# Performance work log

Hardware: AMD Instinct MI355X
Metric: run time of the kernel (lower is better)

The kernel has to match this reference:

```python
import jax, jax.numpy as jnp
import numpy as np
from jax import lax

EMBED = 512
HEADS = 8
KD = EMBED // HEADS  # key_dim == head_dim (value_factor=1)


def setup_inputs() -> dict:
    key = jax.random.key(0)
    ks = jax.random.split(key, 13)
    b, h, w = 4, 128, 128
    s = 0.02
    return {
        "x": jax.random.normal(ks[0], (b, h, w, EMBED), jnp.float32),
        "mask_h": jax.random.normal(ks[1], (HEADS, h, h), jnp.float32),
        "mask_w": jax.random.normal(ks[2], (HEADS, w, w), jnp.float32),
        "Wq": jax.random.normal(ks[3], (EMBED, EMBED), jnp.float32) * s,
        "bq": jnp.zeros((EMBED,), jnp.float32),
        "Wk": jax.random.normal(ks[4], (EMBED, EMBED), jnp.float32) * s,
        "bk": jnp.zeros((EMBED,), jnp.float32),
        "Wv": jax.random.normal(ks[5], (EMBED, EMBED), jnp.float32) * s,
        "bv": jnp.zeros((EMBED,), jnp.float32),
        "lepe_w": jax.random.normal(ks[6], (5, 5, 1, EMBED), jnp.float32) * s,  # depthwise 5x5, HWIO
        "lepe_b": jnp.zeros((EMBED,), jnp.float32),
        "Wo": jax.random.normal(ks[7], (EMBED, EMBED), jnp.float32) * s,
        "bo": jnp.zeros((EMBED,), jnp.float32),
    }


def reference(x, mask_h, mask_w, Wq, bq, Wk, bk, Wv, bv, lepe_w, lepe_b, Wo, bo):
    b, h, w, _ = x.shape
    scaling = KD ** -0.5
    q = x @ Wq + bq                      # (b,h,w,C)
    k = (x @ Wk + bk) * scaling
    v = x @ Wv + bv

    # depthwise-conv positional term (LePE), 5x5 pad 2, groups=C
    lepe = lax.conv_general_dilated(
        v, lepe_w, window_strides=(1, 1), padding=[(2, 2), (2, 2)],
        dimension_numbers=("NHWC", "HWIO", "NHWC"), feature_group_count=EMBED,
    ) + lepe_b

    qr = q.reshape(b, h, w, HEADS, KD)
    kr = k.reshape(b, h, w, HEADS, KD)
    vr = v.reshape(b, h, w, HEADS, KD)

    # width-axis attention (per row), additive per-head decay mask
    sw = jnp.einsum("bhqnd,bhknd->bhnqk", qr, kr) + mask_w[None, None]  # (b,h,n,w,w)
    Aw = jax.nn.softmax(sw, axis=-1)
    o1 = jnp.einsum("bhnqk,bhknd->bhqnd", Aw, vr)                       # (b,h,w,n,d)

    # height-axis attention (per column) on the width-pass output
    sh = jnp.einsum("bqwnd,bkwnd->bwnqk", qr, kr) + mask_h[None, None]  # (b,w,n,h,h)
    Ah = jax.nn.softmax(sh, axis=-1)
    o2 = jnp.einsum("bwnqk,bkwnd->bqwnd", Ah, o1)                       # (b,h,w,n,d)

    out = o2.reshape(b, h, w, EMBED) + lepe
    return out @ Wo + bo
```

## Files before the change

### kernel.cpp

```cpp
#include <hip/hip_runtime.h>
#include <stdint.h>
#include <stddef.h>

typedef unsigned short u16;
typedef __attribute__((ext_vector_type(8))) short bf16x8;
typedef __attribute__((ext_vector_type(4))) float f32x4;

__device__ __forceinline__ u16 f2bf(float f) {
  union { float f; uint32_t u; } v; v.f = f;
  uint32_t u = v.u;
  return (u16)((u + 0x7FFFu + ((u >> 16) & 1u)) >> 16);
}
__device__ __forceinline__ float bf2f(u16 b) {
  union { uint32_t u; float f; } v; v.u = ((uint32_t)b) << 16;
  return v.f;
}

__device__ __forceinline__ void glds16(const u16* g, u16* l) {
  __builtin_amdgcn_global_load_lds((const __attribute__((address_space(1))) void*)g,
                                   (__attribute__((address_space(3))) void*)l, 16, 0, 0);
}

#define MFMA(a, b, c) __builtin_amdgcn_mfma_f32_16x16x32_bf16((a), (b), (c), 0, 0, 0)


__global__ __launch_bounds__(256) void k_cvt_bf16(const float* __restrict__ in,
                                                  u16* __restrict__ out, int n) {
  int i = (blockIdx.x * 256 + threadIdx.x) * 8;
  if (i >= n) return;
  const float4* p = (const float4*)(in + i);
  float4 a = p[0], b = p[1];
  union { bf16x8 v; u16 s[8]; } o;
  o.s[0] = f2bf(a.x); o.s[1] = f2bf(a.y); o.s[2] = f2bf(a.z); o.s[3] = f2bf(a.w);
  o.s[4] = f2bf(b.x); o.s[5] = f2bf(b.y); o.s[6] = f2bf(b.z); o.s[7] = f2bf(b.w);
  *(bf16x8*)(out + i) = o.v;
}


__global__ __launch_bounds__(256) void k_build_w(
    const float* __restrict__ Wq, const float* __restrict__ Wk,
    const float* __restrict__ Wv, const float* __restrict__ Wo,
    const float* __restrict__ bq, const float* __restrict__ bk,
    const float* __restrict__ bv,
    u16* __restrict__ wqkvT, u16* __restrict__ woT, float* __restrict__ bias)
{
  __shared__ u16 tl[64 * 73];
  const int bid = blockIdx.x;
  const int mtx = bid >> 6;
  const int tr = (bid >> 3) & 7, tc = bid & 7;
  const float* W = (mtx == 0) ? Wq : (mtx == 1) ? Wk : (mtx == 2) ? Wv : Wo;
  const float s = (mtx == 1) ? 0.125f : 1.0f;
  const int t = threadIdx.x;
  const int lr = t >> 6, lc = t & 63;
  #pragma unroll
  for (int it = 0; it < 16; ++it) {
    int k = tr * 64 + it * 4 + lr;
    int n = tc * 64 + lc;
    tl[lc * 73 + it * 4 + lr] = f2bf(W[(size_t)k * 512 + n] * s);
  }
  __syncthreads();
  u16* dst = (mtx == 3) ? woT : (wqkvT + (size_t)mtx * 512 * 512);
  #pragma unroll
  for (int it = 0; it < 16; ++it) {
    int n = tc * 64 + it * 4 + lr;
    int k = tr * 64 + lc;
    dst[(size_t)n * 512 + k] = tl[(it * 4 + lr) * 73 + lc];
  }
  if (bid < 6) {
    int i = bid * 256 + t;
    const float* B = (i < 512) ? bq : (i < 1024) ? bk : bv;
    float sc = (i >= 512 && i < 1024) ? 0.125f : 1.0f;
    bias[i] = B[i & 511] * sc;
  }
}


__device__ __forceinline__ void stageH(const u16* __restrict__ src, int ld, size_t grow0,
                                       int kt, int row0, u16* lmat, int t) {
  #pragma unroll
  for (int it = 0; it < 2; ++it) {
    int e = it * 4096 + t * 8;
    int row = row0 + (e >> 6);
    int ch = (e >> 3) & 7;
    int cs = ch ^ (row & 7);
    glds16(src + (grow0 + row) * (size_t)ld + kt * 64 + cs * 8, lmat + row * 64 + ch * 8);
  }
}

__device__ __forceinline__ bf16x8 ldfrag(const u16* lmat, int row, int c) {
  return *(const bf16x8*)(lmat + row * 64 + ((c ^ (row & 7)) << 3));
}

template<bool STAGE, bool VM8>
__device__ __forceinline__ void process_tile(
    const u16* __restrict__ A, int lda, size_t rowA0,
    const u16* __restrict__ BT, int ldb, size_t rowB0,
    u16* LAc, u16* LBc, int nxt,
    int wm, int wn, int fq, int fr, int t,
    f32x4 (&acc)[2][4][2][2])
{
  bf16x8 bA[4][2], bB[2][2][2];
  #pragma unroll
  for (int n = 0; n < 2; ++n)
    #pragma unroll
    for (int kk = 0; kk < 2; ++kk)
      bB[0][n][kk] = ldfrag(LBc, wn * 32 + n * 16 + fr, kk * 4 + fq);
  #pragma unroll
  for (int m = 0; m < 4; ++m)
    #pragma unroll
    for (int kk = 0; kk < 2; ++kk)
      bA[m][kk] = ldfrag(LAc, wm * 64 + m * 16 + fr, kk * 4 + fq);
  __builtin_amdgcn_s_setprio(1);
  #pragma unroll
  for (int m = 0; m < 4; ++m)
    #pragma unroll
    for (int n = 0; n < 2; ++n)
      #pragma unroll
      for (int kk = 0; kk < 2; ++kk)
        acc[0][m][0][n] = MFMA(bA[m][kk], bB[0][n][kk], acc[0][m][0][n]);
  __builtin_amdgcn_s_setprio(0);
  __builtin_amdgcn_s_barrier();
  #pragma unroll
  for (int n = 0; n < 2; ++n)
    #pragma unroll
    for (int kk = 0; kk < 2; ++kk)
      bB[1][n][kk] = ldfrag(LBc, 128 + wn * 32 + n * 16 + fr, kk * 4 + fq);
  if (STAGE) {
    stageH(A, lda, rowA0, nxt, 0, LAc, t);
    stageH(BT, ldb, rowB0, nxt, 0, LBc, t);
  }
  __builtin_amdgcn_s_setprio(1);
  #pragma unroll
  for (int m = 0; m < 4; ++m)
    #pragma unroll
    for (int n = 0; n < 2; ++n)
      #pragma unroll
      for (int kk = 0; kk < 2; ++kk)
        acc[0][m][1][n] = MFMA(bA[m][kk], bB[1][n][kk], acc[0][m][1][n]);
  __builtin_amdgcn_s_setprio(0);
  __builtin_amdgcn_s_barrier();
  #pragma unroll
  for (int m = 0; m < 4; ++m)
    #pragma unroll
    for (int kk = 0; kk < 2; ++kk)
      bA[m][kk] = ldfrag(LAc, 128 + wm * 64 + m * 16 + fr, kk * 4 + fq);
  if (STAGE) stageH(BT, ldb, rowB0, nxt, 128, LBc, t);
  __builtin_amdgcn_s_setprio(1);
  #pragma unroll
  for (int m = 0; m < 4; ++m)
    #pragma unroll
    for (int n = 0; n < 2; ++n)
      #pragma unroll
      for (int kk = 0; kk < 2; ++kk)
        acc[1][m][0][n] = MFMA(bA[m][kk], bB[0][n][kk], acc[1][m][0][n]);
  __builtin_amdgcn_s_setprio(0);
  __builtin_amdgcn_s_barrier();
  if (STAGE) stageH(A, lda, rowA0, nxt, 128, LAc, t);
  __builtin_amdgcn_s_setprio(1);
  #pragma unroll
  for (int m = 0; m < 4; ++m)
    #pragma unroll
    for (int n = 0; n < 2; ++n)
      #pragma unroll
      for (int kk = 0; kk < 2; ++kk)
        acc[1][m][1][n] = MFMA(bA[m][kk], bB[1][n][kk], acc[1][m][1][n]);
  __builtin_amdgcn_s_setprio(0);
  if (VM8) asm volatile("s_waitcnt vmcnt(8)" ::: "memory");
  else     asm volatile("s_waitcnt vmcnt(0)" ::: "memory");
  __builtin_amdgcn_s_barrier();
}

template<bool OUT_F32, int NTN>
__global__ __launch_bounds__(512, 2) void k_gemm256(
    const u16* __restrict__ A, int lda,
    const u16* __restrict__ BT, int ldb,
    const float* __restrict__ bias,
    void* __restrict__ Cp, int ldc)
{
  __shared__ u16 lds[65536];
  u16* LA0 = lds;
  u16* LB0 = lds + 16384;
  u16* LA1 = lds + 32768;
  u16* LB1 = lds + 49152;

  const int t = threadIdx.x, l = t & 63, w = t >> 6;
  const int wm = w >> 2, wn = w & 3;
  const int fq = l >> 4, fr = l & 15;

  const int bid = blockIdx.x;
  const int cpx = gridDim.x >> 3;
  const int swz = (bid & 7) * cpx + (bid >> 3);
  const int tn = swz % NTN, tm = swz / NTN;
  const size_t rowA0 = (size_t)tm * 256;
  const size_t rowB0 = (size_t)tn * 256;

  f32x4 acc[2][4][2][2];
  #pragma unroll
  for (int a = 0; a < 2; ++a)
    #pragma unroll
    for (int m = 0; m < 4; ++m)
      #pragma unroll
      for (int b = 0; b < 2; ++b)
        #pragma unroll
        for (int n = 0; n < 2; ++n) acc[a][m][b][n] = (f32x4){0.f, 0.f, 0.f, 0.f};

  stageH(A,  lda, rowA0, 0, 0,   LA0, t); stageH(A,  lda, rowA0, 0, 128, LA0, t);
  stageH(BT, ldb, rowB0, 0, 0,   LB0, t); stageH(BT, ldb, rowB0, 0, 128, LB0, t);
  stageH(A,  lda, rowA0, 1, 0,   LA1, t); stageH(A,  lda, rowA0, 1, 128, LA1, t);
  stageH(BT, ldb, rowB0, 1, 0,   LB1, t); stageH(BT, ldb, rowB0, 1, 128, LB1, t);
  asm volatile("s_waitcnt vmcnt(8)" ::: "memory");
  __builtin_amdgcn_s_barrier();

  for (int i = 0; i < 3; ++i) {
    process_tile<true, true>(A, lda, rowA0, BT, ldb, rowB0, LA0, LB0, 2 * i + 2,
                             wm, wn, fq, fr, t, acc);
    process_tile<true, true>(A, lda, rowA0, BT, ldb, rowB0, LA1, LB1, 2 * i + 3,
                             wm, wn, fq, fr, t, acc);
  }
  process_tile<false, false>(A, lda, rowA0, BT, ldb, rowB0, LA0, LB0, 0,
                             wm, wn, fq, fr, t, acc);
  process_tile<false, false>(A, lda, rowA0, BT, ldb, rowB0, LA1, LB1, 0,
                             wm, wn, fq, fr, t, acc);

  if (OUT_F32) {
    #pragma unroll
    for (int nh = 0; nh < 2; ++nh)
      #pragma unroll
      for (int n = 0; n < 2; ++n) {
        int col = (int)rowB0 + nh * 128 + wn * 32 + n * 16 + fr;
        float bb = bias[col];
        #pragma unroll
        for (int mh = 0; mh < 2; ++mh)
          #pragma unroll
          for (int m = 0; m < 4; ++m)
            #pragma unroll
            for (int r = 0; r < 4; ++r) {
              size_t row = rowA0 + mh * 128 + wm * 64 + m * 16 + fq * 4 + r;
              ((float*)Cp)[row * ldc + col] = acc[mh][m][nh][n][r] + bb;
            }
      }
  } else {
    #pragma unroll
    for (int mh = 0; mh < 2; ++mh) {
      #pragma unroll
      for (int nh = 0; nh < 2; ++nh)
        #pragma unroll
        for (int n = 0; n < 2; ++n) {
          int col = nh * 128 + wn * 32 + n * 16 + fr;
          float bb = bias[(int)rowB0 + col];
          #pragma unroll
          for (int m = 0; m < 4; ++m)
            #pragma unroll
            for (int r = 0; r < 4; ++r) {
              int row = wm * 64 + m * 16 + fq * 4 + r;
              int ch = (col >> 3) ^ (row & 7);
              lds[row * 256 + ch * 8 + (col & 7)] = f2bf(acc[mh][m][nh][n][r] + bb);
            }
        }
      __syncthreads();
      {
        int row = t >> 2, q = t & 3;
        #pragma unroll
        for (int j = 0; j < 8; ++j) {
          int ch = (q * 8 + j) ^ (row & 7);
          bf16x8 v = *(const bf16x8*)(lds + row * 256 + ch * 8);
          *(bf16x8*)((u16*)Cp + (rowA0 + mh * 128 + row) * (size_t)ldc
                     + rowB0 + q * 64 + j * 8) = v;
        }
      }
      __syncthreads();
    }
  }
}


__global__ __launch_bounds__(256) void k_lepe(
    const u16* __restrict__ qkv, const float* __restrict__ w5,
    const float* __restrict__ lb, u16* __restrict__ outp)
{
  __shared__ u16 wlds[12800];
  #pragma unroll
  for (int j = 0; j < 50; ++j) {
    int idx = j * 256 + threadIdx.x;
    wlds[idx] = f2bf(w5[idx]);
  }
  __syncthreads();

  const int t = threadIdx.x, w = t >> 6, l = t & 63;
  const int c0 = l << 3;
  const int bid = blockIdx.x;
  const int x = (bid & 31) * 4 + w;
  const int y0 = ((bid >> 5) & 15) * 8;
  const int b = bid >> 9;

  float acc[8][8];
  {
    float4 b0 = *(const float4*)(lb + c0);
    float4 b1 = *(const float4*)(lb + c0 + 4);
    #pragma unroll
    for (int tt = 0; tt < 8; ++tt) {
      acc[tt][0] = b0.x; acc[tt][1] = b0.y; acc[tt][2] = b0.z; acc[tt][3] = b0.w;
      acc[tt][4] = b1.x; acc[tt][5] = b1.y; acc[tt][6] = b1.z; acc[tt][7] = b1.w;
    }
  }

  #pragma unroll
  for (int r = 0; r < 12; ++r) {
    int yy = y0 + r - 2;
    if ((unsigned)yy < 128u) {
      #pragma unroll
      for (int dx = 0; dx < 5; ++dx) {
        int xx = x + dx - 2;
        if ((unsigned)xx < 128u) {
          union { bf16x8 v; u16 s[8]; } v8;
          v8.v = *(const bf16x8*)(qkv + (size_t)((b * 128 + yy) * 128 + xx) * 1536
                                  + 1024 + c0);
          float vf[8];
          #pragma unroll
          for (int j = 0; j < 8; ++j) vf[j] = bf2f(v8.s[j]);
          #pragma unroll
          for (int tt = 0; tt < 8; ++tt) {
            int dy = r - tt;
            if (dy >= 0 && dy <= 4) {
              union { bf16x8 v; u16 s[8]; } w8;
              w8.v = *(const bf16x8*)(wlds + (dy * 5 + dx) * 512 + c0);
              #pragma unroll
              for (int j = 0; j < 8; ++j)
                acc[tt][j] += vf[j] * bf2f(w8.s[j]);
            }
          }
        }
      }
    }
  }

  #pragma unroll
  for (int tt = 0; tt < 8; ++tt) {
    size_t tok = (size_t)(b * 128 + y0 + tt) * 128 + x;
    union { bf16x8 v; u16 s[8]; } ov;
    #pragma unroll
    for (int j = 0; j < 8; ++j) ov.s[j] = f2bf(acc[tt][j]);
    *(bf16x8*)(outp + tok * 512 + c0) = ov.v;
  }
}


template<int AXIS>
__global__ __launch_bounds__(512) void k_attn(
    const u16* qkv, const float* __restrict__ mask,
    const u16* __restrict__ lepe, u16* outp)
{
  __shared__ u16 smem[24576];
  u16* q_s = smem;
  u16* k_s = smem + 8192;
  u16* vT  = smem + 16384;
  u16* P   = smem;

  const int t = threadIdx.x, w = t >> 6, l = t & 63;
  const int fq = l >> 4, fr = l & 15;
  const int line = blockIdx.x, head = blockIdx.y, b = blockIdx.z;
  const int coff = head * 64;
  const size_t base0 = (AXIS == 0) ? ((size_t)(b * 128 + line) * 128)
                                   : ((size_t)b * 16384 + line);
  const size_t tstr = (AXIS == 0) ? 1 : 128;

  #pragma unroll
  for (int it = 0; it < 2; ++it) {
    int ee = it * 4096 + t * 8;
    int row = ee >> 6;
    int cs = ((ee >> 3) & 7) ^ (row & 7);
    size_t tok = base0 + (size_t)row * tstr;
    glds16(qkv + tok * 1536 +       coff + cs * 8, q_s + it * 4096 + w * 512);
    glds16(qkv + tok * 1536 + 512 + coff + cs * 8, k_s + it * 4096 + w * 512);
  }
  {
    int chunk = t & 7, kgrp = t >> 3;
    #pragma unroll
    for (int p = 0; p < 2; ++p) {
      int kidx = p * 64 + kgrp;
      size_t tok = base0 + (size_t)kidx * tstr;
      union { bf16x8 v; u16 s[8]; } v8;
      v8.v = *(const bf16x8*)(qkv + tok * 1536 + 1024 + coff + chunk * 8);
      #pragma unroll
      for (int j = 0; j < 8; ++j) {
        int d = chunk * 8 + j;
        int byt = d * 256 + ((2 * kidx) ^ (j << 4) ^ (chunk << 5));
        *(u16*)((char*)vT + byt) = v8.s[j];
      }
    }
  }
  __syncthreads();

  f32x4 acc[8];
  #pragma unroll
  for (int n = 0; n < 8; ++n) acc[n] = (f32x4){0.f, 0.f, 0.f, 0.f};

  #pragma unroll
  for (int kk = 0; kk < 2; ++kk) {
    int arow = w * 16 + fr;
    int ac = (kk * 4 + fq) ^ (arow & 7);
    bf16x8 af = *(const bf16x8*)(q_s + arow * 64 + ac * 8);
    #pragma unroll
    for (int n = 0; n < 8; ++n) {
      int brow = n * 16 + fr;
      int bc = (kk * 4 + fq) ^ (brow & 7);
      bf16x8 bfr = *(const bf16x8*)(k_s + brow * 64 + bc * 8);
      acc[n] = MFMA(af, bfr, acc[n]);
    }
  }

  const float* mbase = mask + (size_t)head * 16384;
  const int q0 = w * 16 + fq * 4;
  #pragma unroll
  for (int n = 0; n < 8; ++n) {
    const float* mp = mbase + (size_t)q0 * 128 + n * 16 + fr;
    #pragma unroll
    for (int r = 0; r < 4; ++r) acc[n][r] += mp[(size_t)r * 128];
  }
  #pragma unroll
  for (int r = 0; r < 4; ++r) {
    float mx = acc[0][r];
    #pragma unroll
    for (int n = 1; n < 8; ++n) mx = fmaxf(mx, acc[n][r]);
    mx = fmaxf(mx, __shfl_xor(mx, 1));
    mx = fmaxf(mx, __shfl_xor(mx, 2));
    mx = fmaxf(mx, __shfl_xor(mx, 4));
    mx = fmaxf(mx, __shfl_xor(mx, 8));
    float sum = 0.f;
    #pragma unroll
    for (int n = 0; n < 8; ++n) {
      float ev = __expf(acc[n][r] - mx);
      acc[n][r] = ev; sum += ev;
    }
    sum += __shfl_xor(sum, 1);
    sum += __shfl_xor(sum, 2);
    sum += __shfl_xor(sum, 4);
    sum += __shfl_xor(sum, 8);
    float inv = 1.0f / sum;
    #pragma unroll
    for (int n = 0; n < 8; ++n) acc[n][r] *= inv;
  }
  __syncthreads();

  #pragma unroll
  for (int r = 0; r < 4; ++r) {
    int row = q0 + r;
    int swz = (row & 7) << 4;
    #pragma unroll
    for (int n = 0; n < 8; ++n) {
      int col = n * 16 + fr;
      *(u16*)((char*)P + row * 256 + ((2 * col) ^ swz)) = f2bf(acc[n][r]);
    }
  }
  __syncthreads();

  f32x4 o[4];
  #pragma unroll
  for (int n = 0; n < 4; ++n) o[n] = (f32x4){0.f, 0.f, 0.f, 0.f};

  #pragma unroll
  for (int kt = 0; kt < 4; ++kt) {
    int arow = w * 16 + fr;
    bf16x8 af = *(const bf16x8*)((const char*)P + arow * 256 +
                 (((kt * 4 + fq) << 4) ^ ((arow & 7) << 4)));
    #pragma unroll
    for (int n = 0; n < 4; ++n) {
      int d = n * 16 + fr;
      int byt = d * 256 + (((kt * 32 + fq * 8) * 2) ^ ((d & 7) << 4)
                           ^ (((d >> 3) & 7) << 5));
      bf16x8 bfr = *(const bf16x8*)((const char*)vT + byt);
      o[n] = MFMA(af, bfr, o[n]);
    }
  }

  #pragma unroll
  for (int r = 0; r < 4; ++r) {
    int i = q0 + r;
    size_t tok = base0 + (size_t)i * tstr;
    #pragma unroll
    for (int n = 0; n < 4; ++n) {
      int d = n * 16 + fr;
      float v = o[n][r];
      if (AXIS == 1) {
        v += bf2f(lepe[tok * 512 + coff + d]);
        outp[tok * 1536 + coff + d] = f2bf(v);
      } else {
        outp[tok * 1536 + 1024 + coff + d] = f2bf(v);
      }
    }
  }
}


extern "C" void kernel_launch(void* const* d_in, const int* in_sizes, int n_in,
                              void* d_out, int out_size, void* d_ws, size_t ws_size,
                              hipStream_t stream) {
  const float* x  = (const float*)d_in[0];
  const float* mh = (const float*)d_in[1];
  const float* mw = (const float*)d_in[2];
  const float* Wq = (const float*)d_in[3];
  const float* bq = (const float*)d_in[4];
  const float* Wk = (const float*)d_in[5];
  const float* bk = (const float*)d_in[6];
  const float* Wv = (const float*)d_in[7];
  const float* bv = (const float*)d_in[8];
  const float* w5 = (const float*)d_in[9];
  const float* lb = (const float*)d_in[10];
  const float* Wo = (const float*)d_in[11];
  const float* bo = (const float*)d_in[12];

  char* ws = (char*)d_ws;
  u16*   qkv   = (u16*)ws;
  u16*   wqkvT = (u16*)(ws + 201326592);
  u16*   woT   = (u16*)(ws + 202899456);
  float* bqkv  = (float*)(ws + 203423744);

  char* od = (char*)d_out;
  u16* xb   = (u16*)od;
  u16* lepe = (u16*)(od + 67108864);

  k_cvt_bf16<<<16384, 256, 0, stream>>>(x, xb, 33554432);
  k_build_w<<<256, 256, 0, stream>>>(Wq, Wk, Wv, Wo, bq, bk, bv, wqkvT, woT, bqkv);

  k_gemm256<false, 6><<<1536, 512, 0, stream>>>(xb, 512, wqkvT, 512, bqkv, qkv, 1536);

  k_lepe<<<2048, 256, 0, stream>>>(qkv, w5, lb, lepe);

  k_attn<0><<<dim3(128, 8, 4), 512, 0, stream>>>(qkv, mw, nullptr, qkv);
  k_attn<1><<<dim3(128, 8, 4), 512, 0, stream>>>(qkv, mh, lepe, qkv);

  k_gemm256<true, 2><<<512, 512, 0, stream>>>(qkv, 1536, woT, 512, bo, d_out, 512);
}
```

Baseline: 465.8 us.

## Write bf16 GEMM epilogue directly to global and split QKV GEMM launch

The bf16 output path of the 256x256 GEMM no longer stages the tile through swizzled LDS with barriers. Each lane now writes its 2-byte results straight to global memory. This drops the LDS round trip and two syncthreads per half-tile, at the cost of narrow scattered stores instead of 16-byte coalesced rows. The QKV projection is also split into two launches over halves of the rows, which may change scheduling and cache behaviour but adds launch overhead.

```diff
diff --git a/kernel.cpp b/kernel.cpp
--- a/kernel.cpp
+++ b/kernel.cpp
@@ -222,55 +222,25 @@
   process_tile<false, false>(A, lda, rowA0, BT, ldb, rowB0, LA1, LB1, 0,
                              wm, wn, fq, fr, t, acc);
 
-  if (OUT_F32) {
-    #pragma unroll
-    for (int nh = 0; nh < 2; ++nh)
-      #pragma unroll
-      for (int n = 0; n < 2; ++n) {
-        int col = (int)rowB0 + nh * 128 + wn * 32 + n * 16 + fr;
-        float bb = bias[col];
+  #pragma unroll
+  for (int nh = 0; nh < 2; ++nh)
+    #pragma unroll
+    for (int n = 0; n < 2; ++n) {
+      int col = (int)rowB0 + nh * 128 + wn * 32 + n * 16 + fr;
+      float bb = bias[col];
+      #pragma unroll
+      for (int mh = 0; mh < 2; ++mh)
         #pragma unroll
-        for (int mh = 0; mh < 2; ++mh)
+        for (int m = 0; m < 4; ++m) {
           #pragma unroll
-          for (int m = 0; m < 4; ++m)
-            #pragma unroll
-            for (int r = 0; r < 4; ++r) {
-              size_t row = rowA0 + mh * 128 + wm * 64 + m * 16 + fq * 4 + r;
-              ((float*)Cp)[row * ldc + col] = acc[mh][m][nh][n][r] + bb;
-            }
-      }
-  } else {
-    #pragma unroll
-    for (int mh = 0; mh < 2; ++mh) {
-      #pragma unroll
-      for (int nh = 0; nh < 2; ++nh)
-        #pragma unroll
-        for (int n = 0; n < 2; ++n) {
-          int col = nh * 128 + wn * 32 + n * 16 + fr;
-          float bb = bias[(int)rowB0 + col];
-          #pragma unroll
-          for (int m = 0; m < 4; ++m)
-            #pragma unroll
-            for (int r = 0; r < 4; ++r) {
-              int row = wm * 64 + m * 16 + fq * 4 + r;
-              int ch = (col >> 3) ^ (row & 7);
-              lds[row * 256 + ch * 8 + (col & 7)] = f2bf(acc[mh][m][nh][n][r] + bb);
-            }
+          for (int r = 0; r < 4; ++r) {
+            size_t row = rowA0 + mh * 128 + wm * 64 + m * 16 + fq * 4 + r;
+            float v = acc[mh][m][nh][n][r] + bb;
+            if (OUT_F32) ((float*)Cp)[row * ldc + col] = v;
+            else         ((u16*)Cp)[row * ldc + col] = f2bf(v);
+          }
         }
-      __syncthreads();
-      {
-        int row = t >> 2, q = t & 3;
-        #pragma unroll
-        for (int j = 0; j < 8; ++j) {
-          int ch = (q * 8 + j) ^ (row & 7);
-          bf16x8 v = *(const bf16x8*)(lds + row * 256 + ch * 8);
-          *(bf16x8*)((u16*)Cp + (rowA0 + mh * 128 + row) * (size_t)ldc
-                     + rowB0 + q * 64 + j * 8) = v;
-        }
-      }
-      __syncthreads();
-    }
-  }
+    }
 }
 
 
@@ -522,7 +492,11 @@
   k_cvt_bf16<<<16384, 256, 0, stream>>>(x, xb, 33554432);
   k_build_w<<<256, 256, 0, stream>>>(Wq, Wk, Wv, Wo, bq, bk, bv, wqkvT, woT, bqkv);
 
-  k_gemm256<false, 6><<<1536, 512, 0, stream>>>(xb, 512, wqkvT, 512, bqkv, qkv, 1536);
+  k_gemm256<false, 6><<<768, 512, 0, stream>>>(xb, 512, wqkvT, 512, bqkv,
+                                               qkv, 1536);
+  k_gemm256<false, 6><<<768, 512, 0, stream>>>(xb + (size_t)32768 * 512, 512,
+                                               wqkvT, 512, bqkv,
+                                               qkv + (size_t)32768 * 1536, 1536);
 
   k_lepe<<<2048, 256, 0, stream>>>(qkv, w5, lb, lepe);
 
```

After: 436.9 us. -6.2%, faster.
